# Kernel tuning notes

Measured on AMD Instinct MI355X. Metric: run time of the kernel, lower is better.

## Reference

```python
import jax, jax.numpy as jnp
import numpy as np

NL, NS, NE = 16, 256, 100   # nlatent, nspatial, n_embd
B, P, T = 2, 2, 12


def _xavier(key, shape):
    # torch xavier_uniform: fan_in = shape[1]*prod(rest), fan_out = shape[0]*prod(rest)
    rf = int(np.prod(shape[2:])) if len(shape) > 2 else 1
    fan_in, fan_out = shape[1] * rf, shape[0] * rf
    b = float(np.sqrt(6.0 / (fan_in + fan_out)))
    return jax.random.uniform(key, shape, jnp.float32, -b, b)


def setup_inputs() -> dict:
    key = jax.random.key(0)
    ks = jax.random.split(key, 8)
    x = jax.random.normal(ks[0], (B, P, T, NL, NS), jnp.float32)
    K = _xavier(ks[1], (NS, NS, NL))
    Q = _xavier(ks[2], (NS, NS, NL))
    V = _xavier(ks[3], (NS, NS, NL))
    Aoo = jnp.ones((NS, NS), jnp.float32)
    # Ann is initialized to zeros in the module; use nonzero values so the
    # clamped geometric recurrence over time is actually exercised.
    Ann = jax.random.uniform(ks[4], (NE,), jnp.float32, -0.9, 0.9)
    Aon = _xavier(ks[5], (NS, NS, NE))
    Ano = _xavier(ks[6], (NS, NS, NE))
    w = jnp.ones((NS,), jnp.float32) / NS
    return {"x": x, "K": K, "Q": Q, "V": V, "Aoo": Aoo,
            "Ann": Ann, "Aon": Aon, "Ano": Ano, "w": w}


def reference(x, K, Q, V, Aoo, Ann, Aon, Ano, w):
    # kvt[B,p,T,X,Y] = sum_{x,c} Q[Y,x,c] K[X,x,c] x[B,p,T,c,x]
    kvt = jnp.einsum('Yxc,Xxc,BpTcx->BpTXY', Q, K, x)
    Aon_c = jnp.clip(Aon, -1.0, 1.0)
    Ano_c = jnp.clip(Ano, -1.0, 1.0)

    # t = T-1 term (elementwise Aoo) and t = T-2 term
    h = Aoo[None, None, None] * kvt[:, :, -1:]
    h = h + jnp.einsum('xyn,XYn,BpTXY->BpTxy', Aon_c, Ano_c, kvt[:, :, -2:-1])

    nT = x.shape[2]
    # Ann sequence used in the loop: A_2 = Ann (raw), A_{j+1} = clip(A_j * Ann)
    def step(a, _):
        return jnp.clip(a * Ann, -1.0, 1.0), a
    _, A_seq = jax.lax.scan(step, Ann, None, length=nT - 2)  # [T-2, n], A_seq[j-2]=A_j

    # loop index j=2..T-1 touches time slice t = T-1-j, i.e. t = T-3 .. 0
    s = jnp.einsum('XYn,BpJXY->BpJn', Ano_c, kvt[:, :, :nT - 2])  # J = t in 0..T-3
    A_t = A_seq[::-1]                       # align A_j with time index t = T-1-j
    s2 = jnp.einsum('Jn,BpJn->Bpn', A_t, s)
    h = h + jnp.einsum('xyn,Bpn->Bpxy', Aon_c, s2)[:, :, None]  # [B,p,1,x,y]

    q = jnp.einsum('Xxc,Bpcx->BpcX', V, x[:, :, -1])
    y = jnp.einsum('x,BpcX,BpTXx->BpTc', w, q, h)  # [B,p,1,c]
    return y
```

## Files before the change

### kernel.cpp

```cpp
#include <hip/hip_runtime.h>
#include <hip/hip_fp16.h>


using f32x4 = __attribute__((ext_vector_type(4))) float;
using half8 = __attribute__((ext_vector_type(8))) _Float16;
using half4 = __attribute__((ext_vector_type(4))) _Float16;

#define KVT_STRIDE 3145728ull
#define KS 4

__device__ inline float clip1(float v) { return fminf(fmaxf(v, -1.f), 1.f); }

__device__ inline half8 mul8(uint4 a, uint4 b) {
    half8 x = __builtin_bit_cast(half8, a);
    half8 y = __builtin_bit_cast(half8, b);
    return x * y;
}

__device__ __forceinline__ void gl_lds16(const void* g, void* l) {
    __builtin_amdgcn_global_load_lds(
        (const __attribute__((address_space(1))) void*)g,
        (__attribute__((address_space(3))) void*)l, 16, 0, 0);
}

__global__ void prep_kernel(const float* __restrict__ K, const float* __restrict__ Q,
                            const float* __restrict__ xin,
                            const float* __restrict__ Aon, const float* __restrict__ wv,
                            const float* __restrict__ V,
                            __half* __restrict__ Kh, __half* __restrict__ Qh,
                            __half* __restrict__ u_t,
                            float* __restrict__ W2p, float* __restrict__ R)
{
    int b = blockIdx.x, t = threadIdx.x;
    if (b < 2048) {
        bool isK = (b < 1024);
        int bb = isK ? b : b - 1024;
        int i = bb * 1024 + t * 4;
        const float4 f = ((const float4*)(isK ? K : Q))[i >> 2];
        half4 v = { (_Float16)f.x, (_Float16)f.y, (_Float16)f.z, (_Float16)f.w };
        *(half4*)((isK ? Kh : Qh) + i) = v;
    } else if (b < 2096) {
        int bt = b - 2048;
        const float* src = xin + (size_t)bt * 4096;
        int xx = t;
        half8 lo, hi;
        #pragma unroll
        for (int c = 0; c < 8; ++c)  lo[c] = (_Float16)src[c * 256 + xx];
        #pragma unroll
        for (int c = 0; c < 8; ++c)  hi[c] = (_Float16)src[(c + 8) * 256 + xx];
        half8* dst = (half8*)(u_t + (size_t)bt * 4096 + xx * 16);
        dst[0] = lo; dst[1] = hi;
    } else if (b < 2608) {
        int idx = b - 2096;
        int X = idx >> 1, h = idx & 1;
        int g = h * 2 + (t >> 7), n = t & 127;
        if (n < 100) {
            const float* base = Aon + (size_t)X * 25600 + (size_t)g * 6400 + n;
            float acc = 0.f;
            for (int bb = 0; bb < 64; ++bb)
                acc += wv[g * 64 + bb] * clip1(__builtin_nontemporal_load(base + (size_t)bb * 100));
            W2p[((size_t)g * 256 + X) * 100 + n] = acc;
        }
    } else {
        __shared__ float vrow[4096];
        int X = b - 2608;
        {
            const float4* src = (const float4*)(V + (size_t)X * 4096);
            float4* dst = (float4*)vrow;
            for (int i = t; i < 1024; i += 256) dst[i] = src[i];
        }
        __syncthreads();
        int bp = t >> 6, c = (t >> 2) & 15, g = t & 3;
        const float* xl = xin + ((size_t)(bp * 12) + 11) * 4096 + c * 256;
        float p = 0.f;
        #pragma unroll 4
        for (int x = g * 64; x < g * 64 + 64; ++x)
            p += xl[x] * vrow[x * 16 + c];
        p += __shfl_xor(p, 1);
        p += __shfl_xor(p, 2);
        if (g == 0) R[((size_t)bp * 256 + X) * 16 + c] = p;
    }
}

__global__ __launch_bounds__(256, 4) void gemm_kvt(
    const __half* __restrict__ Kh, const __half* __restrict__ Qh,
    const __half* __restrict__ u_t, float* __restrict__ kvtp)
{
    __shared__ __half As[2][128][32];
    __shared__ __half Bs[2][128][32];
    __shared__ __half u_s[1024];

    int bid = blockIdx.x;
    int work = (bid & 7) * 96 + (bid >> 3);
    int kc = work / 192;
    int rem = work - kc * 192;
    int tile = rem / 48;
    int bt = rem - tile * 48;
    int Xb = (tile >> 1) * 128, Yb = (tile & 1) * 128;
    int kbase = kc * 1024;

    int tid = threadIdx.x;
    if (tid < 128)
        *(uint4*)&u_s[tid * 8] = *(const uint4*)(u_t + (size_t)bt * 4096 + kbase + tid * 8);
    __syncthreads();

    int wave = tid >> 6, lane = tid & 63;
    int srow = lane >> 2;
    int sk = ((lane & 3) ^ (srow & 3)) * 8;
    const __half* gA = Kh + (size_t)(Xb + wave * 16 + srow) * 4096 + kbase + sk;
    const __half* gB = Qh + (size_t)(Yb + wave * 16 + srow) * 4096 + kbase + sk;

    int wr = (wave >> 1) * 64, wc = (wave & 1) * 64;
    int lrow = lane & 15, kg = lane >> 4;
    int fb = (kg * 16) ^ ((lrow & 3) << 4);

    f32x4 acc[4][4];
    f32x4 zero = {0.f, 0.f, 0.f, 0.f};
    #pragma unroll
    for (int m = 0; m < 4; ++m)
        #pragma unroll
        for (int n = 0; n < 4; ++n) acc[m][n] = zero;

    #define STAGE(s, buf)                                                      \
        do {                                                                   \
            _Pragma("unroll")                                                  \
            for (int i_ = 0; i_ < 2; ++i_) {                                   \
                gl_lds16(gA + (size_t)(i_ * 64) * 4096 + (s) * 32,             \
                         &As[buf][i_ * 64 + wave * 16][0]);                    \
                gl_lds16(gB + (size_t)(i_ * 64) * 4096 + (s) * 32,             \
                         &Bs[buf][i_ * 64 + wave * 16][0]);                    \
            }                                                                  \
        } while (0)

    STAGE(0, 0);
    STAGE(1, 1);

    for (int s = 0; s < 32; ++s) {
        if (s < 31) asm volatile("s_waitcnt vmcnt(4)" ::: "memory");
        else        asm volatile("s_waitcnt vmcnt(0)" ::: "memory");
        __builtin_amdgcn_s_barrier();
        __builtin_amdgcn_sched_barrier(0);

        int cur = s & 1;
        uint4 uv = *(const uint4*)&u_s[s * 32 + kg * 8];
        half8 af[4], bf[4];
        #pragma unroll
        for (int m = 0; m < 4; ++m)
            af[m] = mul8(*(const uint4*)((const char*)&As[cur][wr + m * 16 + lrow][0] + fb), uv);
        #pragma unroll
        for (int n = 0; n < 4; ++n)
            bf[n] = *(const half8*)((const char*)&Bs[cur][wc + n * 16 + lrow][0] + fb);
        #pragma unroll
        for (int m = 0; m < 4; ++m)
            #pragma unroll
            for (int n = 0; n < 4; ++n)
                acc[m][n] = __builtin_amdgcn_mfma_f32_16x16x32_f16(af[m], bf[n], acc[m][n], 0, 0, 0);

        asm volatile("s_waitcnt lgkmcnt(0)" ::: "memory");
        __builtin_amdgcn_s_barrier();
        __builtin_amdgcn_sched_barrier(0);
        if (s + 2 < 32) STAGE(s + 2, cur);
    }
    #undef STAGE

    float* outp = kvtp + (size_t)kc * KVT_STRIDE + (size_t)bt * 65536;
    int row0 = Xb + wr + kg * 4;
    int col0 = Yb + wc + lrow;
    #pragma unroll
    for (int m = 0; m < 4; ++m)
        #pragma unroll
        for (int n = 0; n < 4; ++n)
            #pragma unroll
            for (int rr = 0; rr < 4; ++rr)
                outp[(size_t)(row0 + m * 16 + rr) * 256 + col0 + n * 16] = acc[m][n][rr];
}

__global__ __launch_bounds__(256) void s_partial(const float* __restrict__ Ano,
                                                 const float* __restrict__ kvtp,
                                                 float* __restrict__ Sp)
{
    __shared__ float ano_f[12864];
    __shared__ float kvt_s[44][128];
    int cb = blockIdx.x;
    int k0 = cb * 128;
    int tid = threadIdx.x;

    {
        const f32x4* src = (const f32x4*)(Ano + (size_t)k0 * 100);
        f32x4* dst = (f32x4*)ano_f;
        for (int i = tid; i < 3200; i += 256) {
            f32x4 f = __builtin_nontemporal_load(src + i);
            f.x = clip1(f.x); f.y = clip1(f.y); f.z = clip1(f.z); f.w = clip1(f.w);
            dst[i] = f;
        }
    }
    {
        for (int idx = tid; idx < 5632; idx += 256) {
            int rI = idx >> 7, k = idx & 127;
            int bpr = rI / 11, Jr = rI - bpr * 11;
            size_t off = (size_t)(bpr * 12 + Jr) * 65536 + k0 + k;
            float v = 0.f;
            #pragma unroll
            for (int c = 0; c < KS; ++c) v += kvtp[(size_t)c * KVT_STRIDE + off];
            kvt_s[rI][k] = v;
        }
    }
    __syncthreads();

    int lane = tid & 63;
    int bp = tid >> 6;
    bool has2 = lane < 36;
    float acc0[11], acc1[11];
    #pragma unroll
    for (int J = 0; J < 11; ++J) { acc0[J] = 0.f; acc1[J] = 0.f; }

    for (int k = 0; k < 128; k += 4) {
        f32x4 kv[11];
        #pragma unroll
        for (int J = 0; J < 11; ++J)
            kv[J] = *(const f32x4*)&kvt_s[bp * 11 + J][k];
        #pragma unroll
        for (int kk = 0; kk < 4; ++kk) {
            float a0 = ano_f[(k + kk) * 100 + lane];
            float a1r = ano_f[(k + kk) * 100 + 64 + lane];
            float a1 = has2 ? a1r : 0.f;
            #pragma unroll
            for (int J = 0; J < 11; ++J) {
                acc0[J] += kv[J][kk] * a0;
                acc1[J] += kv[J][kk] * a1;
            }
        }
    }
    float* outb = Sp + ((size_t)cb * 4 + bp) * 1100;
    #pragma unroll
    for (int J = 0; J < 11; ++J) {
        outb[J * 100 + lane] = acc0[J];
        if (has2) outb[J * 100 + 64 + lane] = acc1[J];
    }
}

__global__ void reduce_s(const float* __restrict__ Sp, float* __restrict__ Sq)
{
    int bid = blockIdx.x;
    int qq = bid & 3, idx = bid >> 2;
    int bp = idx / 11, J = idx - bp * 11;
    int t = threadIdx.x;
    if (t >= 100) return;
    float acc = 0.f;
    for (int c = qq * 128; c < qq * 128 + 128; ++c)
        acc += Sp[((size_t)c * 4 + bp) * 1100 + J * 100 + t];
    Sq[(size_t)(qq * 44 + idx) * 100 + t] = acc;
}

__global__ void c2_kernel(const float* __restrict__ Sq, const float* __restrict__ Ann,
                          float* __restrict__ c2, float* __restrict__ out)
{
    int t = threadIdx.x;
    if (t < 64) out[t] = 0.f;
    int bp = t >> 7, n = t & 127;
    if (n >= 100) return;
    float S[11];
    #pragma unroll
    for (int J = 0; J < 11; ++J) {
        float s = 0.f;
        #pragma unroll
        for (int qq = 0; qq < 4; ++qq)
            s += Sq[(size_t)(qq * 44 + bp * 11 + J) * 100 + n];
        S[J] = s;
    }
    float a = Ann[n];
    float seq[10];
    float v = a;
    seq[0] = v;
    #pragma unroll
    for (int s = 1; s < 10; ++s) { v = clip1(v * a); seq[s] = v; }
    float r = S[10];
    #pragma unroll
    for (int J = 0; J < 10; ++J)
        r += seq[9 - J] * S[J];
    c2[bp * 100 + n] = r;
}

__global__ __launch_bounds__(256) void hw_kernel(const float* __restrict__ Aoo,
                                                 const float* __restrict__ wv,
                                                 const float* __restrict__ kvtp,
                                                 const float* __restrict__ W2p,
                                                 const float* __restrict__ c2,
                                                 const float* __restrict__ R,
                                                 float* __restrict__ out)
{
    __shared__ float yp[4][16];
    int bp = blockIdx.x >> 6, Xg = blockIdx.x & 63;
    int tid = threadIdx.x;
    int wave = tid >> 6, lane = tid & 63;
    int X = Xg * 4 + wave;
    size_t base = (size_t)(bp * 12 + 11) * 65536 + (size_t)X * 256;
    const float* ao = Aoo + (size_t)X * 256;
    float red = 0.f;
    #pragma unroll
    for (int qq = 0; qq < 4; ++qq) {
        int xx = qq * 64 + lane;
        float kvv = 0.f;
        #pragma unroll
        for (int c = 0; c < KS; ++c) kvv += kvtp[(size_t)c * KVT_STRIDE + base + xx];
        red += wv[xx] * ao[xx] * kvv;
    }
    float w2a = 0.f, w2b = 0.f;
    #pragma unroll
    for (int g = 0; g < 4; ++g) {
        w2a += W2p[((size_t)g * 256 + X) * 100 + lane];
        if (lane < 36) w2b += W2p[((size_t)g * 256 + X) * 100 + 64 + lane];
    }
    red += c2[bp * 100 + lane] * w2a;
    if (lane < 36)
        red += c2[bp * 100 + 64 + lane] * w2b;
    #pragma unroll
    for (int off = 32; off; off >>= 1) red += __shfl_xor(red, off);
    if (lane < 16) yp[wave][lane] = red * R[((size_t)bp * 256 + X) * 16 + lane];
    __syncthreads();
    if (tid < 16) {
        float s = yp[0][tid] + yp[1][tid] + yp[2][tid] + yp[3][tid];
        atomicAdd(&out[bp * 16 + tid], s);
    }
}

extern "C" void kernel_launch(void* const* d_in, const int* in_sizes, int n_in,
                              void* d_out, int out_size, void* d_ws, size_t ws_size,
                              hipStream_t stream)
{
    const float* x   = (const float*)d_in[0];
    const float* K   = (const float*)d_in[1];
    const float* Q   = (const float*)d_in[2];
    const float* V   = (const float*)d_in[3];
    const float* Aoo = (const float*)d_in[4];
    const float* Ann = (const float*)d_in[5];
    const float* Aon = (const float*)d_in[6];
    const float* Ano = (const float*)d_in[7];
    const float* wv  = (const float*)d_in[8];
    float* out = (float*)d_out;

    char* ws = (char*)d_ws;
    const size_t o_Qh   = 0;
    const size_t o_Kh   = o_Qh + (size_t)2 * 1024 * 1024;
    const size_t o_ut   = o_Kh + (size_t)2 * 1024 * 1024;
    const size_t o_kvtp = o_ut + (size_t)512 * 1024;
    const size_t o_Sp   = o_kvtp + (size_t)KS * KVT_STRIDE * 4;
    const size_t o_Sq   = o_Sp + (size_t)512 * 4400 * 4;
    const size_t o_c2   = o_Sq + (size_t)17600 * 4;
    const size_t o_W2   = o_c2 + 400 * 4 + 64;
    const size_t o_R    = o_W2 + (size_t)102400 * 4;

    __half* Qh  = (__half*)(ws + o_Qh);
    __half* Kh  = (__half*)(ws + o_Kh);
    __half* u_t = (__half*)(ws + o_ut);
    float* kvtp = (float*)(ws + o_kvtp);
    float* Sp   = (float*)(ws + o_Sp);
    float* Sq   = (float*)(ws + o_Sq);
    float* c2   = (float*)(ws + o_c2);
    float* W2p  = (float*)(ws + o_W2);
    float* R    = (float*)(ws + o_R);

    hipLaunchKernelGGL(prep_kernel, dim3(2864), dim3(256), 0, stream,
                       K, Q, x, Aon, wv, V, Kh, Qh, u_t, W2p, R);
    hipLaunchKernelGGL(gemm_kvt,    dim3(768),  dim3(256), 0, stream, Kh, Qh, u_t, kvtp);
    hipLaunchKernelGGL(s_partial,   dim3(512),  dim3(256), 0, stream, Ano, kvtp, Sp);
    hipLaunchKernelGGL(reduce_s,    dim3(176),  dim3(128), 0, stream, Sp, Sq);
    hipLaunchKernelGGL(c2_kernel,   dim3(1),    dim3(512), 0, stream, Sq, Ann, c2, out);
    hipLaunchKernelGGL(hw_kernel,   dim3(256),  dim3(256), 0, stream,
                       Aoo, wv, kvtp, W2p, c2, R, out);
}
```

Measured before the change: 109.0 us.

## Store kvt partials in fp16, fold c2 into hw_kernel, retune LDS swizzle

Split-K partial results of the kvt GEMM are now written as half precision instead of fp32, halving the write traffic from gemm_kvt and the read traffic in s_partial and hw_kernel. The single-block c2 kernel is removed: each hw_kernel block recomputes c2 into shared memory, and the output zeroing moves into reduce_s, saving one launch. The LDS XOR swizzle pattern also changes to use row bits shifted by one. The costs are precision loss on the stored partials and redundant c2 computation in every hw block.

```diff
diff --git a/kernel.cpp b/kernel.cpp
--- a/kernel.cpp
+++ b/kernel.cpp
@@ -84,7 +84,7 @@
 
 __global__ __launch_bounds__(256, 4) void gemm_kvt(
     const __half* __restrict__ Kh, const __half* __restrict__ Qh,
-    const __half* __restrict__ u_t, float* __restrict__ kvtp)
+    const __half* __restrict__ u_t, __half* __restrict__ kvtp)
 {
     __shared__ __half As[2][128][32];
     __shared__ __half Bs[2][128][32];
@@ -106,13 +106,13 @@
 
     int wave = tid >> 6, lane = tid & 63;
     int srow = lane >> 2;
-    int sk = ((lane & 3) ^ (srow & 3)) * 8;
+    int sk = ((lane & 3) ^ ((srow >> 1) & 3)) << 3;
     const __half* gA = Kh + (size_t)(Xb + wave * 16 + srow) * 4096 + kbase + sk;
     const __half* gB = Qh + (size_t)(Yb + wave * 16 + srow) * 4096 + kbase + sk;
 
     int wr = (wave >> 1) * 64, wc = (wave & 1) * 64;
     int lrow = lane & 15, kg = lane >> 4;
-    int fb = (kg * 16) ^ ((lrow & 3) << 4);
+    int fb = (kg * 16) ^ (((lrow >> 1) & 3) << 4);
 
     f32x4 acc[4][4];
     f32x4 zero = {0.f, 0.f, 0.f, 0.f};
@@ -163,7 +163,7 @@
     }
     #undef STAGE
 
-    float* outp = kvtp + (size_t)kc * KVT_STRIDE + (size_t)bt * 65536;
+    __half* outp = kvtp + (size_t)kc * KVT_STRIDE + (size_t)bt * 65536;
     int row0 = Xb + wr + kg * 4;
     int col0 = Yb + wc + lrow;
     #pragma unroll
@@ -172,11 +172,12 @@
         for (int n = 0; n < 4; ++n)
             #pragma unroll
             for (int rr = 0; rr < 4; ++rr)
-                outp[(size_t)(row0 + m * 16 + rr) * 256 + col0 + n * 16] = acc[m][n][rr];
+                outp[(size_t)(row0 + m * 16 + rr) * 256 + col0 + n * 16] =
+                    __float2half(acc[m][n][rr]);
 }
 
 __global__ __launch_bounds__(256) void s_partial(const float* __restrict__ Ano,
-                                                 const float* __restrict__ kvtp,
+                                                 const __half* __restrict__ kvtp,
                                                  float* __restrict__ Sp)
 {
     __shared__ float ano_f[12864];
@@ -201,7 +202,8 @@
             size_t off = (size_t)(bpr * 12 + Jr) * 65536 + k0 + k;
             float v = 0.f;
             #pragma unroll
-            for (int c = 0; c < KS; ++c) v += kvtp[(size_t)c * KVT_STRIDE + off];
+            for (int c = 0; c < KS; ++c)
+                v += __half2float(kvtp[(size_t)c * KVT_STRIDE + off]);
             kvt_s[rI][k] = v;
         }
     }
@@ -239,12 +241,14 @@
     }
 }
 
-__global__ void reduce_s(const float* __restrict__ Sp, float* __restrict__ Sq)
+__global__ void reduce_s(const float* __restrict__ Sp, float* __restrict__ Sq,
+                         float* __restrict__ out)
 {
     int bid = blockIdx.x;
+    int t = threadIdx.x;
+    if (bid == 0 && t < 64) out[t] = 0.f;
     int qq = bid & 3, idx = bid >> 2;
     int bp = idx / 11, J = idx - bp * 11;
-    int t = threadIdx.x;
     if (t >= 100) return;
     float acc = 0.f;
     for (int c = qq * 128; c < qq * 128 + 128; ++c)
@@ -252,46 +256,48 @@
     Sq[(size_t)(qq * 44 + idx) * 100 + t] = acc;
 }
 
-__global__ void c2_kernel(const float* __restrict__ Sq, const float* __restrict__ Ann,
-                          float* __restrict__ c2, float* __restrict__ out)
-{
-    int t = threadIdx.x;
-    if (t < 64) out[t] = 0.f;
-    int bp = t >> 7, n = t & 127;
-    if (n >= 100) return;
-    float S[11];
-    #pragma unroll
-    for (int J = 0; J < 11; ++J) {
-        float s = 0.f;
-        #pragma unroll
-        for (int qq = 0; qq < 4; ++qq)
-            s += Sq[(size_t)(qq * 44 + bp * 11 + J) * 100 + n];
-        S[J] = s;
-    }
-    float a = Ann[n];
-    float seq[10];
-    float v = a;
-    seq[0] = v;
-    #pragma unroll
-    for (int s = 1; s < 10; ++s) { v = clip1(v * a); seq[s] = v; }
-    float r = S[10];
-    #pragma unroll
-    for (int J = 0; J < 10; ++J)
-        r += seq[9 - J] * S[J];
-    c2[bp * 100 + n] = r;
-}
-
 __global__ __launch_bounds__(256) void hw_kernel(const float* __restrict__ Aoo,
                                                  const float* __restrict__ wv,
-                                                 const float* __restrict__ kvtp,
+                                                 const __half* __restrict__ kvtp,
                                                  const float* __restrict__ W2p,
-                                                 const float* __restrict__ c2,
+                                                 const float* __restrict__ Sq,
+                                                 const float* __restrict__ Ann,
                                                  const float* __restrict__ R,
                                                  float* __restrict__ out)
 {
     __shared__ float yp[4][16];
+    __shared__ float c2s[128];
     int bp = blockIdx.x >> 6, Xg = blockIdx.x & 63;
     int tid = threadIdx.x;
+
+    if (tid < 128) {
+        int n = tid;
+        float r = 0.f;
+        if (n < 100) {
+            float S[11];
+            #pragma unroll
+            for (int J = 0; J < 11; ++J) {
+                float s = 0.f;
+                #pragma unroll
+                for (int qq = 0; qq < 4; ++qq)
+                    s += Sq[(size_t)(qq * 44 + bp * 11 + J) * 100 + n];
+                S[J] = s;
+            }
+            float a = Ann[n];
+            float seq[10];
+            float v = a;
+            seq[0] = v;
+            #pragma unroll
+            for (int s2 = 1; s2 < 10; ++s2) { v = clip1(v * a); seq[s2] = v; }
+            r = S[10];
+            #pragma unroll
+            for (int J = 0; J < 10; ++J)
+                r += seq[9 - J] * S[J];
+        }
+        c2s[n] = r;
+    }
+    __syncthreads();
+
     int wave = tid >> 6, lane = tid & 63;
     int X = Xg * 4 + wave;
     size_t base = (size_t)(bp * 12 + 11) * 65536 + (size_t)X * 256;
@@ -302,7 +308,8 @@
         int xx = qq * 64 + lane;
         float kvv = 0.f;
         #pragma unroll
-        for (int c = 0; c < KS; ++c) kvv += kvtp[(size_t)c * KVT_STRIDE + base + xx];
+        for (int c = 0; c < KS; ++c)
+            kvv += __half2float(kvtp[(size_t)c * KVT_STRIDE + base + xx]);
         red += wv[xx] * ao[xx] * kvv;
     }
     float w2a = 0.f, w2b = 0.f;
@@ -311,9 +318,9 @@
         w2a += W2p[((size_t)g * 256 + X) * 100 + lane];
         if (lane < 36) w2b += W2p[((size_t)g * 256 + X) * 100 + 64 + lane];
     }
-    red += c2[bp * 100 + lane] * w2a;
+    red += c2s[lane] * w2a;
     if (lane < 36)
-        red += c2[bp * 100 + 64 + lane] * w2b;
+        red += c2s[64 + lane] * w2b;
     #pragma unroll
     for (int off = 32; off; off >>= 1) red += __shfl_xor(red, off);
     if (lane < 16) yp[wave][lane] = red * R[((size_t)bp * 256 + X) * 16 + lane];
@@ -344,19 +351,17 @@
     const size_t o_Kh   = o_Qh + (size_t)2 * 1024 * 1024;
     const size_t o_ut   = o_Kh + (size_t)2 * 1024 * 1024;
     const size_t o_kvtp = o_ut + (size_t)512 * 1024;
-    const size_t o_Sp   = o_kvtp + (size_t)KS * KVT_STRIDE * 4;
+    const size_t o_Sp   = o_kvtp + (size_t)KS * KVT_STRIDE * 2;
     const size_t o_Sq   = o_Sp + (size_t)512 * 4400 * 4;
-    const size_t o_c2   = o_Sq + (size_t)17600 * 4;
-    const size_t o_W2   = o_c2 + 400 * 4 + 64;
+    const size_t o_W2   = o_Sq + (size_t)17600 * 4 + 64;
     const size_t o_R    = o_W2 + (size_t)102400 * 4;
 
     __half* Qh  = (__half*)(ws + o_Qh);
     __half* Kh  = (__half*)(ws + o_Kh);
     __half* u_t = (__half*)(ws + o_ut);
-    float* kvtp = (float*)(ws + o_kvtp);
+    __half* kvtp = (__half*)(ws + o_kvtp);
     float* Sp   = (float*)(ws + o_Sp);
     float* Sq   = (float*)(ws + o_Sq);
-    float* c2   = (float*)(ws + o_c2);
     float* W2p  = (float*)(ws + o_W2);
     float* R    = (float*)(ws + o_R);
 
@@ -364,8 +369,7 @@
                        K, Q, x, Aon, wv, V, Kh, Qh, u_t, W2p, R);
     hipLaunchKernelGGL(gemm_kvt,    dim3(768),  dim3(256), 0, stream, Kh, Qh, u_t, kvtp);
     hipLaunchKernelGGL(s_partial,   dim3(512),  dim3(256), 0, stream, Ano, kvtp, Sp);
-    hipLaunchKernelGGL(reduce_s,    dim3(176),  dim3(128), 0, stream, Sp, Sq);
-    hipLaunchKernelGGL(c2_kernel,   dim3(1),    dim3(512), 0, stream, Sq, Ann, c2, out);
+    hipLaunchKernelGGL(reduce_s,    dim3(176),  dim3(128), 0, stream, Sp, Sq, out);
     hipLaunchKernelGGL(hw_kernel,   dim3(256),  dim3(256), 0, stream,
-                       Aoo, wv, kvtp, W2p, c2, R, out);
-}
+                       Aoo, wv, kvtp, W2p, Sq, Ann, R, out);
+}
```

After: 105.1 us (median of 2 runs). 1.04x faster.
